# Performance work log

Measured on AMD Instinct MI355X. Metric: run time of the kernel, lower is better.

## Reference

```python
import jax, jax.numpy as jnp
import numpy as np

B, N, D, H, C = 1, 256, 128, 4, 32  # batch, n_res, d_pair, n_head, c


def setup_inputs() -> dict:
    key = jax.random.key(0)
    ks = jax.random.split(key, 5)
    s = 1.0 / np.sqrt(D)
    return {
        "Z_raw": jax.random.normal(ks[0], (B, N, N, D), jnp.float32),
        "Z_mask": jnp.ones((B, N, N), jnp.float32),
        "ln_gamma": jnp.ones((D,), jnp.float32),
        "ln_beta": jnp.zeros((D,), jnp.float32),
        "w_b": jax.random.normal(ks[1], (H, D), jnp.float32) * s,
        "w_qkv": jax.random.normal(ks[2], (3 * H * C, D), jnp.float32) * s,
        "w_g": jax.random.normal(ks[3], (H * C, D), jnp.float32) * s,
        "b_g": jnp.ones((H * C,), jnp.float32),
        "w_o": jax.random.normal(ks[4], (D, H * C), jnp.float32) * (1.0 / np.sqrt(H * C)),
        "out_bias": jnp.zeros((D,), jnp.float32),
    }


def reference(Z_raw, Z_mask, ln_gamma, ln_beta, w_b, w_qkv, w_g, b_g, w_o, out_bias):
    # ending-node: transpose the two residue axes
    Z = jnp.swapaxes(Z_raw, 1, 2)            # [B, I, J, D]
    mask = jnp.swapaxes(Z_mask, 1, 2)        # [B, I, J]
    # LayerNorm over channels
    mu = jnp.mean(Z, axis=-1, keepdims=True)
    var = jnp.mean(jnp.square(Z - mu), axis=-1, keepdims=True)
    Zn = (Z - mu) * jax.lax.rsqrt(var + 1e-5) * ln_gamma + ln_beta
    # pair bias: [B, H, q, k]
    b = jnp.einsum('bqkd,hd->bhqk', Zn, w_b)
    # fused qkv projection (no bias)
    qkv = jnp.einsum('bijd,ed->bije', Zn, w_qkv)      # e = 3*H*C
    q, k, v = jnp.split(qkv, 3, axis=-1)
    heads = lambda t: jnp.transpose(t.reshape(B, N, N, H, C), (0, 1, 3, 2, 4))  # [B,I,H,J,C]
    q = heads(q) * (C ** -0.5)
    k = heads(k)
    v = heads(v)
    logits = jnp.einsum('bihqc,bihkc->bihqk', q, k)
    logits = logits + (1e9 * (mask - 1.0))[:, :, None, None, :] + b[:, None]
    w = jax.nn.softmax(logits, axis=-1)
    o = jnp.einsum('bihqk,bihkc->bihqc', w, v)
    o = jnp.transpose(o, (0, 1, 3, 2, 4)).reshape(B, N, N, H * C)
    # sigmoid gating (weight zero-init in torch; here random, bias init ones)
    g = jax.nn.sigmoid(jnp.einsum('bijd,ed->bije', Zn, w_g) + b_g)
    o = jnp.einsum('bije,de->bijd', g * o, w_o)       # output linear, bias fused out
    # transpose back + fused bias-dropout-add (eval: dropout is identity, mask ones)
    return jnp.swapaxes(o, 1, 2) + out_bias + Z_raw
```

## Files before the change

### kernel.cpp

```cpp
#include <hip/hip_runtime.h>

typedef __attribute__((ext_vector_type(4))) float  f32x4;
typedef __attribute__((ext_vector_type(8))) short  bf16x8;
typedef __attribute__((ext_vector_type(4))) int    i32x4;
typedef __attribute__((ext_vector_type(2))) unsigned short u16x2;
typedef __attribute__((ext_vector_type(4))) unsigned short u16x4;
typedef __attribute__((ext_vector_type(2))) unsigned int   u32x2;

#define ZN_OFF    0u
#define QSEP_OFF  16777216u
#define KSEP_OFF  33554432u
#define GBUF_OFF  50331648u
#define VT_OFF    67108864u
#define BIAS_OFF  83886080u
#define WCAT_OFF  84934656u
#define WO_OFF    85066752u

__device__ __forceinline__ unsigned short f2bf(float x){
  unsigned int u = __builtin_bit_cast(unsigned int, x);
  unsigned int r = (u + 0x7FFFu + ((u>>16)&1u)) >> 16;
  return (unsigned short)r;
}
__device__ __forceinline__ float bf2f(unsigned short b){
  unsigned int u = ((unsigned int)b) << 16;
  return __builtin_bit_cast(float, u);
}
__device__ __forceinline__ f32x4 fmax4(f32x4 a, f32x4 b){
  f32x4 r; r[0]=fmaxf(a[0],b[0]); r[1]=fmaxf(a[1],b[1]);
  r[2]=fmaxf(a[2],b[2]); r[3]=fmaxf(a[3],b[3]); return r;
}
__device__ __forceinline__ unsigned packbf2(float lo, float hi){
  return __builtin_amdgcn_perm(__builtin_bit_cast(unsigned, hi),
                               __builtin_bit_cast(unsigned, lo), 0x07060302u);
}

__global__ __launch_bounds__(256) void prep_ln_kernel(
    const float* __restrict__ Z_raw, const float* __restrict__ ln_gamma,
    const float* __restrict__ ln_beta,
    const float* __restrict__ w_qkv, const float* __restrict__ w_g,
    const float* __restrict__ w_b,  const float* __restrict__ w_o,
    unsigned short* __restrict__ Zn, unsigned short* __restrict__ Wcat,
    unsigned short* __restrict__ Wo_bf)
{
  if (blockIdx.x >= 8192){
    int idx = (blockIdx.x - 8192)*256 + threadIdx.x;
    if (idx < 516*128){
      int r = idx >> 7, d = idx & 127;
      float v;
      if (r < 384)      v = w_qkv[idx];
      else if (r < 512) v = w_g[(r-384)*128 + d];
      else              v = w_b[(r-512)*128 + d];
      if (r < 128) v *= 0.17677669529663689f;
      Wcat[idx] = f2bf(v);
    } else if (idx < 516*128 + 128*128){
      int k = idx - 516*128;
      Wo_bf[k] = f2bf(w_o[k]);
    }
    return;
  }
  int wid = threadIdx.x >> 6, lane = threadIdx.x & 63;
  int half = lane >> 5, l32 = lane & 31;
  int n = blockIdx.x*8 + wid*2 + half;
  int i = n & 255, j = n >> 8;
  int m = i*256 + j;
  f32x4 v = *reinterpret_cast<const f32x4*>(&Z_raw[((size_t)(j*256 + i))*128 + l32*4]);
  float s  = (v[0]+v[1]) + (v[2]+v[3]);
  float sq = (v[0]*v[0]+v[1]*v[1]) + (v[2]*v[2]+v[3]*v[3]);
  #pragma unroll
  for (int mk=1; mk<32; mk<<=1){ s += __shfl_xor(s, mk, 64); sq += __shfl_xor(sq, mk, 64); }
  float mu   = s * (1.0f/128.0f);
  float var  = sq*(1.0f/128.0f) - mu*mu;
  float rstd = rsqrtf(var + 1e-5f);
  f32x4 g4 = *reinterpret_cast<const f32x4*>(&ln_gamma[l32*4]);
  f32x4 b4 = *reinterpret_cast<const f32x4*>(&ln_beta[l32*4]);
  u16x4 o;
  #pragma unroll
  for (int t=0; t<4; ++t) o[t] = f2bf((v[t]-mu)*rstd*g4[t] + b4[t]);
  *reinterpret_cast<u16x4*>(&Zn[(size_t)m*128 + l32*4]) = o;
}

__global__ __launch_bounds__(256) void gemm_qkvg_kernel(
    const unsigned short* __restrict__ Zn, const unsigned short* __restrict__ Wcat,
    unsigned short* __restrict__ Qsep, unsigned short* __restrict__ Ksep,
    unsigned short* __restrict__ Gbuf, unsigned short* __restrict__ Vt,
    float* __restrict__ bias4)
{
  __shared__ __align__(16) char sA[32768];
  __shared__ __align__(16) char sB[32768];
  int rb = blockIdx.x;
  int t = threadIdx.x;
  const char* gA = (const char*)Zn + (size_t)rb*32768;
  #pragma unroll
  for (int it=0; it<8; ++it){
    int off = it*4096 + t*16;
    int row = off >> 8;
    int swz = off ^ ((row&7)<<4);
    *reinterpret_cast<i32x4*>(sA + swz) = *reinterpret_cast<const i32x4*>(gA + off);
    *reinterpret_cast<i32x4*>(sB + swz) = *reinterpret_cast<const i32x4*>((const char*)Wcat + off);
  }
  __syncthreads();
  int wid = t>>6, lane = t&63;
  int wr = wid>>1, wc = wid&1;
  int lcol = lane & 15, lk16 = (lane>>4)*16;
  int r0 = (lane>>4)*4, hi = lane>>4;

  #pragma unroll
  for (int cb=0; cb<4; ++cb){
    f32x4 acc[4][4] = {};
    #pragma unroll
    for (int ks=0; ks<4; ++ks){
      bf16x8 a[4], b[4];
      #pragma unroll
      for (int mi=0; mi<4; ++mi){
        int row = wr*64 + mi*16 + lcol;
        int off = row*256 + ks*64 + lk16;
        a[mi] = *reinterpret_cast<const bf16x8*>(sA + (off ^ ((row&7)<<4)));
      }
      #pragma unroll
      for (int ni=0; ni<4; ++ni){
        int row = wc*64 + ni*16 + lcol;
        int off = row*256 + ks*64 + lk16;
        b[ni] = *reinterpret_cast<const bf16x8*>(sB + (off ^ ((row&7)<<4)));
      }
      #pragma unroll
      for (int mi=0; mi<4; ++mi)
        #pragma unroll
        for (int ni=0; ni<4; ++ni)
          acc[mi][ni] = __builtin_amdgcn_mfma_f32_16x16x32_bf16(a[mi], b[ni], acc[mi][ni], 0,0,0);
    }
    if (cb <= 1){
      unsigned short* __restrict__ dst = cb ? Ksep : Qsep;
      #pragma unroll
      for (int mi=0; mi<4; ++mi)
        #pragma unroll
        for (int ni=0; ni<4; ++ni){
          int e = wc*64 + ni*16 + lcol;
          int hh = e>>5, c = e&31;
          int mrow = rb*128 + wr*64 + mi*16 + r0;
          #pragma unroll
          for (int r=0; r<4; ++r){
            int m = mrow + r;
            int i2 = m >> 8, j2 = m & 255;
            dst[(size_t)((i2*4 + hh)*256 + j2)*32 + c] = f2bf(acc[mi][ni][r]);
          }
        }
      if (cb == 0){
        bf16x8 wb[4];
        #pragma unroll
        for (int ks=0; ks<4; ++ks){
          if (lcol < 4)
            wb[ks] = *reinterpret_cast<const bf16x8*>(&Wcat[(512+lcol)*128 + ks*32 + hi*8]);
          else
            wb[ks] = (bf16x8){0,0,0,0,0,0,0,0};
        }
        #pragma unroll
        for (int sti=0; sti<2; ++sti){
          int st = wid*2 + sti;
          f32x4 accb = {0.f,0.f,0.f,0.f};
          #pragma unroll
          for (int ks=0; ks<4; ++ks){
            int row = st*16 + lcol;
            int off = row*256 + ks*64 + lk16;
            bf16x8 a = *reinterpret_cast<const bf16x8*>(sA + (off ^ ((row&7)<<4)));
            accb = __builtin_amdgcn_mfma_f32_16x16x32_bf16(a, wb[ks], accb, 0,0,0);
          }
          if (lcol < 4){
            int mr = rb*128 + st*16 + hi*4;
            int i2 = mr >> 8, jb = mr & 255;
            *reinterpret_cast<f32x4*>(&bias4[((size_t)(lcol*64 + (jb>>2))*256 + i2)*4]) = accb;
          }
        }
      }
    } else if (cb == 3){
      #pragma unroll
      for (int mi=0; mi<4; ++mi)
        #pragma unroll
        for (int ni=0; ni<4; ++ni){
          int col = wc*64 + ni*16 + lcol;
          int mrow = rb*128 + wr*64 + mi*16 + r0;
          #pragma unroll
          for (int r=0; r<4; ++r)
            Gbuf[(size_t)(mrow+r)*128 + col] = f2bf(acc[mi][ni][r]);
        }
    } else {
      #pragma unroll
      for (int mi=0; mi<4; ++mi)
        #pragma unroll
        for (int ni=0; ni<4; ++ni){
          int e = wc*64 + ni*16 + lcol;
          int hh = e>>5, c = e&31;
          int mrow = rb*128 + wr*64 + mi*16 + r0;
          int i2 = mrow >> 8, j2 = mrow & 255;
          u16x4 pk;
          #pragma unroll
          for (int r=0; r<4; ++r) pk[r] = f2bf(acc[mi][ni][r]);
          *reinterpret_cast<u16x4*>(&Vt[(size_t)((i2*4 + hh)*32 + c)*256 + j2]) = pk;
        }
    }
    if (cb < 3){
      __syncthreads();
      #pragma unroll
      for (int it=0; it<8; ++it){
        int off = it*4096 + t*16;
        int row = off >> 8;
        int swz = off ^ ((row&7)<<4);
        *reinterpret_cast<i32x4*>(sB + swz) =
          *reinterpret_cast<const i32x4*>((const char*)Wcat + (cb+1)*32768 + off);
      }
      __syncthreads();
    }
  }
}

__global__ __launch_bounds__(256, 2) void attn_kernel(
    const unsigned short* __restrict__ Qsep, const unsigned short* __restrict__ Ksep,
    const unsigned short* __restrict__ Vt, const float* __restrict__ bias4,
    const float* __restrict__ Z_mask, unsigned short* __restrict__ o_buf)
{
  __shared__ __align__(16) char sK[16384];
  __shared__ __align__(16) char sV[16384];
  __shared__ __align__(16) char sP[4096];
  __shared__ float smask[256];
  int ia = blockIdx.x >> 2, h = blockIdx.x & 3;
  int t = threadIdx.x;
  {
    const char* srcK = (const char*)&Ksep[(size_t)((ia*4 + h)*256)*32];
    const char* srcV = (const char*)&Vt[(size_t)((ia*4 + h)*32)*256];
    #pragma unroll
    for (int it=0; it<4; ++it){
      int off = (it*256 + t)*16;
      int rowK = off >> 6;
      *reinterpret_cast<i32x4*>(sK + (off ^ ((rowK&7)<<4))) =
        *reinterpret_cast<const i32x4*>(srcK + off);
      int rowV = off >> 9;
      *reinterpret_cast<i32x4*>(sV + (off ^ ((rowV&7)<<4))) =
        *reinterpret_cast<const i32x4*>(srcV + off);
    }
  }
  smask[t] = 1e9f * (Z_mask[(size_t)t*256 + ia] - 1.0f);
  __syncthreads();

  int wid = t>>6, lane = t&63;
  int lq = lane & 15;
  int hi = lane >> 4;
  char* sPw = sP + wid*1024;
  int pswz = (lq&7)<<4;
  const f32x4* b4 = reinterpret_cast<const f32x4*>(bias4);

  #pragma unroll 1
  for (int mi=0; mi<4; ++mi){
    int q0 = wid*64 + mi*16;
    int q  = q0 + lq;
    bf16x8 aq = *reinterpret_cast<const bf16x8*>(
        &Qsep[(size_t)((ia*4 + h)*256 + q)*32 + hi*8]);
    f32x4 oacc[2] = {};
    float mrun = 0.f, lsum = 0.f;
    #pragma unroll 1
    for (int half=0; half<2; ++half){
      f32x4 s[8];
      #pragma unroll
      for (int ni=0; ni<8; ++ni){
        int g  = half*32 + ni*4 + hi;
        int k0 = half*128 + ni*16 + hi*4;
        f32x4 bb  = b4[(size_t)(h*64 + g)*256 + q];
        f32x4 msk = *reinterpret_cast<const f32x4*>(&smask[k0]);
        s[ni] = bb + msk;
      }
      #pragma unroll
      for (int ni=0; ni<8; ++ni){
        int krow = half*128 + ni*16 + lq;
        int off  = krow*64 + hi*16;
        bf16x8 bk = *reinterpret_cast<const bf16x8*>(sK + (off ^ ((krow&7)<<4)));
        s[ni] = __builtin_amdgcn_mfma_f32_16x16x32_bf16(bk, aq, s[ni], 0,0,0);
      }
      f32x4 m4 = fmax4(s[0], s[1]);
      m4 = fmax4(m4, fmax4(s[2], s[3]));
      m4 = fmax4(m4, fmax4(s[4], s[5]));
      m4 = fmax4(m4, fmax4(s[6], s[7]));
      float mx = fmaxf(fmaxf(m4[0], m4[1]), fmaxf(m4[2], m4[3]));
      mx = fmaxf(mx, __shfl_xor(mx, 16, 64));
      mx = fmaxf(mx, __shfl_xor(mx, 32, 64));
      if (half == 0){
        mrun = mx;
      } else {
        float mnew = fmaxf(mrun, mx);
        float sc = __expf(mrun - mnew);
        lsum *= sc;
        mrun = mnew;
        #pragma unroll
        for (int r=0; r<4; ++r){
          float scr = __shfl(sc, hi*4 + r, 64);
          oacc[0][r] *= scr;
          oacc[1][r] *= scr;
        }
      }
      f32x4 sum4 = {0.f,0.f,0.f,0.f};
      #pragma unroll
      for (int ni=0; ni<8; ++ni){
        f32x4 p;
        #pragma unroll
        for (int r=0; r<4; ++r) p[r] = __expf(s[ni][r] - mrun);
        s[ni] = p;
        sum4 += p;
      }
      lsum += (sum4[0]+sum4[1]) + (sum4[2]+sum4[3]);
      #pragma unroll
      for (int ck=0; ck<4; ++ck){
        #pragma unroll
        for (int nl=0; nl<2; ++nl){
          int ni = ck*2 + nl;
          u32x2 w;
          w.x = packbf2(s[ni][0], s[ni][1]);
          w.y = packbf2(s[ni][2], s[ni][3]);
          *reinterpret_cast<u32x2*>(sPw + ((lq*64 + nl*32 + hi*8) ^ pswz)) = w;
        }
        bf16x8 ap = *reinterpret_cast<const bf16x8*>(sPw + ((lq*64 + hi*16) ^ pswz));
        int ks = half*4 + ck;
        #pragma unroll
        for (int nc=0; nc<2; ++nc){
          int vrow = nc*16 + lq;
          int voff = vrow*512 + ks*64 + hi*16;
          bf16x8 bv = *reinterpret_cast<const bf16x8*>(sV + (voff ^ ((vrow&7)<<4)));
          oacc[nc] = __builtin_amdgcn_mfma_f32_16x16x32_bf16(ap, bv, oacc[nc], 0,0,0);
        }
      }
    }
    float sum = lsum;
    sum += __shfl_xor(sum, 16, 64);
    sum += __shfl_xor(sum, 32, 64);
    float rinv[4];
    #pragma unroll
    for (int r=0; r<4; ++r)
      rinv[r] = __builtin_amdgcn_rcpf(__shfl(sum, hi*4 + r, 64));
    #pragma unroll
    for (int nc=0; nc<2; ++nc)
      #pragma unroll
      for (int r=0; r<4; ++r){
        int qo = q0 + hi*4 + r;
        o_buf[(size_t)(ia*256 + qo)*128 + h*32 + nc*16 + lq] = f2bf(oacc[nc][r] * rinv[r]);
      }
  }
}

__global__ __launch_bounds__(256) void final_kernel(
    const unsigned short* __restrict__ Gbuf, const unsigned short* __restrict__ o_buf,
    const unsigned short* __restrict__ Wo_bf, const float* __restrict__ b_g,
    const float* __restrict__ out_bias, const float* __restrict__ Z_raw,
    float* __restrict__ out)
{
  __shared__ __align__(16) char sA[32768];
  __shared__ __align__(16) char sB[32768];
  int rb = blockIdx.x, t = threadIdx.x;
  #pragma unroll
  for (int it=0; it<8; ++it){
    int idx = (it*256 + t)*8;
    int row = idx >> 7, e0 = idx & 127;
    size_t m = (size_t)rb*128 + row;
    bf16x8 gv = *reinterpret_cast<const bf16x8*>(&Gbuf[m*128 + e0]);
    bf16x8 ov = *reinterpret_cast<const bf16x8*>(&o_buf[m*128 + e0]);
    bf16x8 av;
    #pragma unroll
    for (int jj=0; jj<8; ++jj){
      float g  = bf2f((unsigned short)gv[jj]) + b_g[e0+jj];
      float sg = 1.0f/(1.0f + __expf(-g));
      av[jj] = (short)f2bf(sg * bf2f((unsigned short)ov[jj]));
    }
    int off = idx*2;
    *reinterpret_cast<bf16x8*>(sA + (off ^ ((row&7)<<4))) = av;
    *reinterpret_cast<i32x4*>(sB + (off ^ ((row&7)<<4))) =
      *reinterpret_cast<const i32x4*>(&Wo_bf[idx]);
  }
  __syncthreads();
  int wid = t>>6, lane = t&63;
  int wr = wid>>1, wc = wid&1;
  int lcol = lane & 15, lk16 = (lane>>4)*16;
  f32x4 acc[4][4] = {};
  #pragma unroll
  for (int ks=0; ks<4; ++ks){
    bf16x8 a[4], b[4];
    #pragma unroll
    for (int mi=0; mi<4; ++mi){
      int row = wr*64 + mi*16 + lcol;
      int off = row*256 + ks*64 + lk16;
      a[mi] = *reinterpret_cast<const bf16x8*>(sA + (off ^ ((row&7)<<4)));
    }
    #pragma unroll
    for (int ni=0; ni<4; ++ni){
      int row = wc*64 + ni*16 + lcol;
      int off = row*256 + ks*64 + lk16;
      b[ni] = *reinterpret_cast<const bf16x8*>(sB + (off ^ ((row&7)<<4)));
    }
    #pragma unroll
    for (int mi=0; mi<4; ++mi)
      #pragma unroll
      for (int ni=0; ni<4; ++ni)
        acc[mi][ni] = __builtin_amdgcn_mfma_f32_16x16x32_bf16(a[mi], b[ni], acc[mi][ni], 0,0,0);
  }
  int r0 = (lane>>4)*4;
  #pragma unroll
  for (int mi=0; mi<4; ++mi)
    #pragma unroll
    for (int ni=0; ni<4; ++ni){
      int col = wc*64 + ni*16 + lcol;
      #pragma unroll
      for (int r=0; r<4; ++r){
        int mrow = rb*128 + wr*64 + mi*16 + r0 + r;
        int i = mrow >> 8, j = mrow & 255;
        size_t oidx = ((size_t)(j*256 + i))*128 + col;
        out[oidx] = acc[mi][ni][r] + out_bias[col] + Z_raw[oidx];
      }
    }
}

extern "C" void kernel_launch(void* const* d_in, const int* in_sizes, int n_in,
                              void* d_out, int out_size, void* d_ws, size_t ws_size,
                              hipStream_t stream)
{
  (void)in_sizes; (void)n_in; (void)out_size; (void)ws_size;
  const float* Z_raw    = (const float*)d_in[0];
  const float* Z_mask   = (const float*)d_in[1];
  const float* ln_gamma = (const float*)d_in[2];
  const float* ln_beta  = (const float*)d_in[3];
  const float* w_b      = (const float*)d_in[4];
  const float* w_qkv    = (const float*)d_in[5];
  const float* w_g      = (const float*)d_in[6];
  const float* b_g      = (const float*)d_in[7];
  const float* w_o      = (const float*)d_in[8];
  const float* out_bias = (const float*)d_in[9];
  float* out = (float*)d_out;

  char* ws = (char*)d_ws;
  unsigned short* Zn    = (unsigned short*)(ws + ZN_OFF);
  unsigned short* Qsep  = (unsigned short*)(ws + QSEP_OFF);
  unsigned short* Ksep  = (unsigned short*)(ws + KSEP_OFF);
  unsigned short* Gbuf  = (unsigned short*)(ws + GBUF_OFF);
  unsigned short* Vt    = (unsigned short*)(ws + VT_OFF);
  float*          biasb = (float*)(ws + BIAS_OFF);
  unsigned short* Wcat  = (unsigned short*)(ws + WCAT_OFF);
  unsigned short* Wo_bf = (unsigned short*)(ws + WO_OFF);
  unsigned short* o_buf = Zn;

  prep_ln_kernel<<<dim3(8514), dim3(256), 0, stream>>>(
      Z_raw, ln_gamma, ln_beta, w_qkv, w_g, w_b, w_o, Zn, Wcat, Wo_bf);
  gemm_qkvg_kernel<<<dim3(512), dim3(256), 0, stream>>>(
      Zn, Wcat, Qsep, Ksep, Gbuf, Vt, biasb);
  attn_kernel<<<dim3(1024), dim3(256), 0, stream>>>(Qsep, Ksep, Vt, biasb, Z_mask, o_buf);
  final_kernel<<<dim3(512), dim3(256), 0, stream>>>(Gbuf, o_buf, Wo_bf, b_g, out_bias, Z_raw, out);
}
```

Measured before the change: 91.37 us.

## Move sigmoid gating into QKV GEMM epilogue and attention output; add MFMA priority hints

The sigmoid gate (with its bias) is now computed in the QKV/G GEMM epilogue and stored in a head-separated layout. The attention kernel multiplies its normalized output by the gate before writing. The final kernel then loads the gated activations straight into shared memory, with no elementwise sigmoid work in its prologue. s_setprio hints are also placed around the MFMA loops in attention, so waves in their matrix phase get scheduling priority. The cost is an extra strided bf16 gate load per output element in attention, plus an expf per element in the GEMM epilogue.

```diff
diff --git a/kernel.cpp b/kernel.cpp
--- a/kernel.cpp
+++ b/kernel.cpp
@@ -10,7 +10,7 @@
 #define ZN_OFF    0u
 #define QSEP_OFF  16777216u
 #define KSEP_OFF  33554432u
-#define GBUF_OFF  50331648u
+#define GSEP_OFF  50331648u
 #define VT_OFF    67108864u
 #define BIAS_OFF  83886080u
 #define WCAT_OFF  84934656u
@@ -81,8 +81,9 @@
 
 __global__ __launch_bounds__(256) void gemm_qkvg_kernel(
     const unsigned short* __restrict__ Zn, const unsigned short* __restrict__ Wcat,
+    const float* __restrict__ b_g,
     unsigned short* __restrict__ Qsep, unsigned short* __restrict__ Ksep,
-    unsigned short* __restrict__ Gbuf, unsigned short* __restrict__ Vt,
+    unsigned short* __restrict__ Gsep, unsigned short* __restrict__ Vt,
     float* __restrict__ bias4)
 {
   __shared__ __align__(16) char sA[32768];
@@ -128,8 +129,8 @@
         for (int ni=0; ni<4; ++ni)
           acc[mi][ni] = __builtin_amdgcn_mfma_f32_16x16x32_bf16(a[mi], b[ni], acc[mi][ni], 0,0,0);
     }
-    if (cb <= 1){
-      unsigned short* __restrict__ dst = cb ? Ksep : Qsep;
+    if (cb != 2){
+      unsigned short* __restrict__ dst = (cb==0) ? Qsep : (cb==1 ? Ksep : Gsep);
       #pragma unroll
       for (int mi=0; mi<4; ++mi)
         #pragma unroll
@@ -141,7 +142,12 @@
           for (int r=0; r<4; ++r){
             int m = mrow + r;
             int i2 = m >> 8, j2 = m & 255;
-            dst[(size_t)((i2*4 + hh)*256 + j2)*32 + c] = f2bf(acc[mi][ni][r]);
+            float val = acc[mi][ni][r];
+            if (cb == 3){
+              float gl = val + b_g[e];
+              val = 1.0f/(1.0f + __expf(-gl));
+            }
+            dst[(size_t)((i2*4 + hh)*256 + j2)*32 + c] = f2bf(val);
           }
         }
       if (cb == 0){
@@ -171,17 +177,6 @@
           }
         }
       }
-    } else if (cb == 3){
-      #pragma unroll
-      for (int mi=0; mi<4; ++mi)
-        #pragma unroll
-        for (int ni=0; ni<4; ++ni){
-          int col = wc*64 + ni*16 + lcol;
-          int mrow = rb*128 + wr*64 + mi*16 + r0;
-          #pragma unroll
-          for (int r=0; r<4; ++r)
-            Gbuf[(size_t)(mrow+r)*128 + col] = f2bf(acc[mi][ni][r]);
-        }
     } else {
       #pragma unroll
       for (int mi=0; mi<4; ++mi)
@@ -214,8 +209,9 @@
 
 __global__ __launch_bounds__(256, 2) void attn_kernel(
     const unsigned short* __restrict__ Qsep, const unsigned short* __restrict__ Ksep,
-    const unsigned short* __restrict__ Vt, const float* __restrict__ bias4,
-    const float* __restrict__ Z_mask, unsigned short* __restrict__ o_buf)
+    const unsigned short* __restrict__ Vt, const unsigned short* __restrict__ Gsep,
+    const float* __restrict__ bias4, const float* __restrict__ Z_mask,
+    unsigned short* __restrict__ o_buf)
 {
   __shared__ __align__(16) char sK[16384];
   __shared__ __align__(16) char sV[16384];
@@ -266,6 +262,7 @@
         f32x4 msk = *reinterpret_cast<const f32x4*>(&smask[k0]);
         s[ni] = bb + msk;
       }
+      __builtin_amdgcn_s_setprio(1);
       #pragma unroll
       for (int ni=0; ni<8; ++ni){
         int krow = half*128 + ni*16 + lq;
@@ -273,6 +270,7 @@
         bf16x8 bk = *reinterpret_cast<const bf16x8*>(sK + (off ^ ((krow&7)<<4)));
         s[ni] = __builtin_amdgcn_mfma_f32_16x16x32_bf16(bk, aq, s[ni], 0,0,0);
       }
+      __builtin_amdgcn_s_setprio(0);
       f32x4 m4 = fmax4(s[0], s[1]);
       m4 = fmax4(m4, fmax4(s[2], s[3]));
       m4 = fmax4(m4, fmax4(s[4], s[5]));
@@ -304,6 +302,7 @@
         sum4 += p;
       }
       lsum += (sum4[0]+sum4[1]) + (sum4[2]+sum4[3]);
+      __builtin_amdgcn_s_setprio(1);
       #pragma unroll
       for (int ck=0; ck<4; ++ck){
         #pragma unroll
@@ -324,6 +323,7 @@
           oacc[nc] = __builtin_amdgcn_mfma_f32_16x16x32_bf16(ap, bv, oacc[nc], 0,0,0);
         }
       }
+      __builtin_amdgcn_s_setprio(0);
     }
     float sum = lsum;
     sum += __shfl_xor(sum, 16, 64);
@@ -337,38 +337,29 @@
       #pragma unroll
       for (int r=0; r<4; ++r){
         int qo = q0 + hi*4 + r;
-        o_buf[(size_t)(ia*256 + qo)*128 + h*32 + nc*16 + lq] = f2bf(oacc[nc][r] * rinv[r]);
+        float gv = bf2f(Gsep[(size_t)((ia*4 + h)*256 + qo)*32 + nc*16 + lq]);
+        o_buf[(size_t)(ia*256 + qo)*128 + h*32 + nc*16 + lq] =
+            f2bf(oacc[nc][r] * rinv[r] * gv);
       }
   }
 }
 
 __global__ __launch_bounds__(256) void final_kernel(
-    const unsigned short* __restrict__ Gbuf, const unsigned short* __restrict__ o_buf,
-    const unsigned short* __restrict__ Wo_bf, const float* __restrict__ b_g,
+    const unsigned short* __restrict__ o_buf, const unsigned short* __restrict__ Wo_bf,
     const float* __restrict__ out_bias, const float* __restrict__ Z_raw,
     float* __restrict__ out)
 {
   __shared__ __align__(16) char sA[32768];
   __shared__ __align__(16) char sB[32768];
   int rb = blockIdx.x, t = threadIdx.x;
+  const char* gO = (const char*)o_buf + (size_t)rb*32768;
   #pragma unroll
   for (int it=0; it<8; ++it){
-    int idx = (it*256 + t)*8;
-    int row = idx >> 7, e0 = idx & 127;
-    size_t m = (size_t)rb*128 + row;
-    bf16x8 gv = *reinterpret_cast<const bf16x8*>(&Gbuf[m*128 + e0]);
-    bf16x8 ov = *reinterpret_cast<const bf16x8*>(&o_buf[m*128 + e0]);
-    bf16x8 av;
-    #pragma unroll
-    for (int jj=0; jj<8; ++jj){
-      float g  = bf2f((unsigned short)gv[jj]) + b_g[e0+jj];
-      float sg = 1.0f/(1.0f + __expf(-g));
-      av[jj] = (short)f2bf(sg * bf2f((unsigned short)ov[jj]));
-    }
-    int off = idx*2;
-    *reinterpret_cast<bf16x8*>(sA + (off ^ ((row&7)<<4))) = av;
-    *reinterpret_cast<i32x4*>(sB + (off ^ ((row&7)<<4))) =
-      *reinterpret_cast<const i32x4*>(&Wo_bf[idx]);
+    int off = it*4096 + t*16;
+    int row = off >> 8;
+    int swz = off ^ ((row&7)<<4);
+    *reinterpret_cast<i32x4*>(sA + swz) = *reinterpret_cast<const i32x4*>(gO + off);
+    *reinterpret_cast<i32x4*>(sB + swz) = *reinterpret_cast<const i32x4*>((const char*)Wo_bf + off);
   }
   __syncthreads();
   int wid = t>>6, lane = t&63;
@@ -433,7 +424,7 @@
   unsigned short* Zn    = (unsigned short*)(ws + ZN_OFF);
   unsigned short* Qsep  = (unsigned short*)(ws + QSEP_OFF);
   unsigned short* Ksep  = (unsigned short*)(ws + KSEP_OFF);
-  unsigned short* Gbuf  = (unsigned short*)(ws + GBUF_OFF);
+  unsigned short* Gsep  = (unsigned short*)(ws + GSEP_OFF);
   unsigned short* Vt    = (unsigned short*)(ws + VT_OFF);
   float*          biasb = (float*)(ws + BIAS_OFF);
   unsigned short* Wcat  = (unsigned short*)(ws + WCAT_OFF);
@@ -443,7 +434,8 @@
   prep_ln_kernel<<<dim3(8514), dim3(256), 0, stream>>>(
       Z_raw, ln_gamma, ln_beta, w_qkv, w_g, w_b, w_o, Zn, Wcat, Wo_bf);
   gemm_qkvg_kernel<<<dim3(512), dim3(256), 0, stream>>>(
-      Zn, Wcat, Qsep, Ksep, Gbuf, Vt, biasb);
-  attn_kernel<<<dim3(1024), dim3(256), 0, stream>>>(Qsep, Ksep, Vt, biasb, Z_mask, o_buf);
-  final_kernel<<<dim3(512), dim3(256), 0, stream>>>(Gbuf, o_buf, Wo_bf, b_g, out_bias, Z_raw, out);
-}
+      Zn, Wcat, b_g, Qsep, Ksep, Gsep, Vt, biasb);
+  attn_kernel<<<dim3(1024), dim3(256), 0, stream>>>(
+      Qsep, Ksep, Vt, Gsep, biasb, Z_mask, o_buf);
+  final_kernel<<<dim3(512), dim3(256), 0, stream>>>(o_buf, Wo_bf, out_bias, Z_raw, out);
+}
```

After: 86.00 us. 5.9% less time.
